# Optimization experiments

Measured on AMD Instinct MI355X. Metric: run time of the kernel, lower is better.

## Reference

```python
import jax, jax.numpy as jnp
import numpy as np

N, T, D, C = 32, 512, 1024, 120
EPS = 1e-12
SCALE = 2.0 * (D ** 0.5)


def setup_inputs() -> dict:
    key = jax.random.key(0)
    ks = jax.random.split(key, 16)
    inp = {
        'anc_perm_input': jax.random.normal(ks[0], (N, T, D), dtype=jnp.float32),
        'pos_perm_input': jax.random.normal(ks[1], (N, T, D), dtype=jnp.float32),
        'neg_perm_input': jax.random.normal(ks[2], (N, T, D), dtype=jnp.float32),
        'anc_src_key_padding_mask': jax.random.randint(ks[3], (N, T), 0, 2) == 1,
        'pos_src_key_padding_mask': jax.random.randint(ks[4], (N, T), 0, 2) == 1,
        'neg_src_key_padding_mask': jax.random.randint(ks[5], (N, T), 0, 2) == 1,
        # learned parameters (stored as (in, out); math-equivalent to torch x @ W.T)
        'W_attn': jax.random.normal(ks[6], (D, D), dtype=jnp.float32) * 0.02,
        'b_attn': jnp.zeros((D,), dtype=jnp.float32),
        'W1': jax.random.normal(ks[7], (D, D), dtype=jnp.float32) * 0.02,
        'b1': jnp.zeros((D,), dtype=jnp.float32),
        'W2': jax.random.normal(ks[8], (D, D), dtype=jnp.float32) * 0.02,
        'b2': jnp.zeros((D,), dtype=jnp.float32),
        'ln_g': jnp.ones((D,), dtype=jnp.float32),
        'ln_b': jnp.zeros((D,), dtype=jnp.float32),
        'W_last': jax.random.normal(ks[9], (D, C), dtype=jnp.float32) * 0.02,
        'b_last': jnp.zeros((C,), dtype=jnp.float32),
    }
    return inp


def _ntd_nd(x, mask, W_attn, b_attn, W1, b1, W2, b2, ln_g, ln_b, W_last, b_last):
    # x: (N,T,D); mask: (N,T) bool, True = padding
    w = x @ W_attn + b_attn                                   # (N,T,D)
    valid = ~mask                                             # (N,T)
    scores = jnp.einsum('btd,bsd->bts', w, w)                 # (N,T,T)
    scores = jnp.where(valid[:, :, None] & valid[:, None, :], scores, 0.0)
    s = jnp.sum(scores, axis=1) / SCALE                       # (N,T)
    s = jnp.where(mask, -jnp.inf, s)
    attn = jax.nn.softmax(s, axis=1)                          # (N,T)
    # proj_head: duplicate OrderedDict key => linear1 -> relu -> linear2 (no final act)
    proj = jax.nn.relu(x @ W1 + b1) @ W2 + b2                 # (N,T,D)
    pooled = jnp.einsum('bt,btd->bd', attn, proj)             # (N,D)
    mu = jnp.mean(pooled, axis=-1, keepdims=True)
    var = jnp.var(pooled, axis=-1, keepdims=True)
    normed = (pooled - mu) / jnp.sqrt(var + EPS) * ln_g + ln_b
    return jax.nn.relu(normed) @ W_last + b_last              # (N,C)


def reference(anc_perm_input, pos_perm_input, neg_perm_input,
              anc_src_key_padding_mask, pos_src_key_padding_mask, neg_src_key_padding_mask,
              W_attn, b_attn, W1, b1, W2, b2, ln_g, ln_b, W_last, b_last):
    params = (W_attn, b_attn, W1, b1, W2, b2, ln_g, ln_b, W_last, b_last)
    anc = _ntd_nd(anc_perm_input, anc_src_key_padding_mask, *params)
    pos = _ntd_nd(pos_perm_input, pos_src_key_padding_mask, *params)
    neg = _ntd_nd(neg_perm_input, neg_src_key_padding_mask, *params)
    return (anc, pos, neg)
```

## Files before the change

### kernel.cpp

```cpp
#include <hip/hip_runtime.h>
#include <hip/hip_bf16.h>
#include <math.h>

#define N_B 32
#define T_S 512
#define D_D 1024
#define C_C 120
#define ZB 96
#define SCALE 64.0f

typedef unsigned short u16;
typedef __attribute__((ext_vector_type(8))) short short8;
typedef __attribute__((ext_vector_type(8))) unsigned short ushort8;
typedef __attribute__((ext_vector_type(4))) float floatx4;

__device__ inline u16 f2bf(float f) {
    union { __hip_bfloat16 h; u16 u; } c; c.h = __float2bfloat16(f); return c.u;
}
__device__ inline float bf2f(u16 u) {
    union { unsigned i; float f; } c; c.i = ((unsigned)u) << 16; return c.f;
}

__device__ inline void gll16(const void* g, void* l) {
    __builtin_amdgcn_global_load_lds((const __attribute__((address_space(1))) void*)g,
                                     (__attribute__((address_space(3))) void*)l,
                                     16, 0, 0);
}

__device__ inline bool mask_is_i8(const int* mk) {
    bool i8 = false;
#pragma unroll
    for (int i = 0; i < 16; i++) {
        unsigned v = ((const unsigned*)mk)[i];
        if (v > 1u) i8 = true;
    }
    return i8;
}
__device__ inline int mask_val(const int* mk, int idx, bool i8) {
    return i8 ? (int)((const signed char*)mk)[idx] : mk[idx];
}

__global__ __launch_bounds__(512)
void k_scan(const int* m0, const int* m1, const int* m2,
            int* __restrict__ slotbase, int* __restrict__ cnts,
            int* __restrict__ gb, int* __restrict__ zblk,
            int* __restrict__ mtot, u16* __restrict__ xp,
            float* __restrict__ attnw, float4* __restrict__ zreg) {
    int zb = blockIdx.x;
    int tid = threadIdx.x;
    {
        float4 zz4 = {0.f, 0.f, 0.f, 0.f};
        for (int i = zb * 512 + tid; i < (2 * 1024 * 1024 / 16); i += ZB * 512)
            zreg[i] = zz4;
    }
    bool i8_0 = mask_is_i8(m0), i8_1 = mask_is_i8(m1), i8_2 = mask_is_i8(m2);
    __shared__ unsigned short wc[ZB][8];
    __shared__ int scnt[ZB], sgb[ZB], stot;
    int wave = tid >> 6, lane = tid & 63;
#pragma unroll
    for (int it = 0; it < 12; it++) {
        int zb2 = wave * 12 + it;
        int z2 = zb2 >> 5, b2 = zb2 & 31;
        const int* mk = z2 == 0 ? m0 : (z2 == 1 ? m1 : m2);
        bool i8 = z2 == 0 ? i8_0 : (z2 == 1 ? i8_1 : i8_2);
        int c = 0;
        if (i8) {
            const signed char* p = (const signed char*)mk + b2 * T_S + lane * 8;
#pragma unroll
            for (int e = 0; e < 8; e++) c += (p[e] == 0);
        } else {
            const int* p = mk + b2 * T_S + lane * 8;
#pragma unroll
            for (int e = 0; e < 8; e++) c += (p[e] == 0);
        }
        c += __shfl_xor(c, 1, 64);
        c += __shfl_xor(c, 2, 64);
        c += __shfl_xor(c, 4, 64);
        if ((lane & 7) == 0) wc[zb2][lane >> 3] = (unsigned short)c;
    }
    __syncthreads();
    if (tid < ZB) {
        int s = 0;
#pragma unroll
        for (int c = 0; c < 8; c++) s += wc[tid][c];
        scnt[tid] = s;
    }
    __syncthreads();
    if (tid == 0) {
        int run = 0;
        for (int i = 0; i < ZB; i++) { sgb[i] = run; run += (scnt[i] + 63) & ~63; }
        stot = run;
    }
    __syncthreads();
    int cnt = scnt[zb], base = sgb[zb];
    if (tid == 0) {
        cnts[zb] = cnt; gb[zb] = base;
        int run = base;
#pragma unroll
        for (int c = 0; c < 8; c++) { slotbase[zb * 8 + c] = run; run += wc[zb][c]; }
        if (zb == ZB - 1) mtot[0] = stot;
    }
    int nb = (cnt + 63) >> 6;
    if (tid < nb) zblk[(base >> 6) + tid] = zb;
    int cend = (cnt + 63) & ~63;
    {
        u16* bp = xp + (size_t)(base + cnt) * D_D;
        int n8 = (cend - cnt) * (D_D / 8);
        ushort8 zz = {0,0,0,0,0,0,0,0};
        for (int i = tid; i < n8; i += 512)
            *(ushort8*)(bp + (size_t)i * 8) = zz;
    }
    if (zb == ZB - 1) {
        int tot = stot, tend = (tot + 255) & ~255;
        u16* bp = xp + (size_t)tot * D_D;
        int n8 = (tend - tot) * (D_D / 8);
        ushort8 zz = {0,0,0,0,0,0,0,0};
        for (int i = tid; i < n8; i += 512)
            *(ushort8*)(bp + (size_t)i * 8) = zz;
        for (int i = tid; i < tend - tot; i += 512) attnw[tot + i] = 0.f;
        if (tid < ((tend - tot) >> 6)) zblk[(tot >> 6) + tid] = 0;
    }
}

__global__ void k_prep(const float* __restrict__ W_attn, const float* __restrict__ W1,
                       const float* x0, const float* x1, const float* x2,
                       const int* m0, const int* m1, const int* m2,
                       const int* __restrict__ slotbase,
                       float* __restrict__ WT, u16* __restrict__ W1T,
                       float* __restrict__ xsum, u16* __restrict__ xp) {
    int bx = blockIdx.x;
    int tid = threadIdx.x;
    if (bx < 1024) {
        int tbx = bx & 31, tby = bx >> 5;
        __shared__ float tile[32][33];
        int tx = tid & 31, ty = tid >> 5;
#pragma unroll
        for (int j = 0; j < 32; j += 8)
            tile[ty + j][tx] = W_attn[(size_t)(tby*32 + ty + j)*D_D + tbx*32 + tx];
        __syncthreads();
#pragma unroll
        for (int j = 0; j < 32; j += 8)
            WT[(size_t)(tbx*32 + ty + j)*D_D + tby*32 + tx] = tile[tx][ty + j];
        __syncthreads();
#pragma unroll
        for (int j = 0; j < 32; j += 8)
            tile[ty + j][tx] = W1[(size_t)(tby*32 + ty + j)*D_D + tbx*32 + tx];
        __syncthreads();
#pragma unroll
        for (int j = 0; j < 32; j += 8)
            W1T[(size_t)(tbx*32 + ty + j)*D_D + tby*32 + tx] = f2bf(tile[tx][ty + j]);
        return;
    }
    int idx = bx - 1024;
    int chunk = idx & 7, zb = idx >> 3;
    int z = zb >> 5, b = zb & 31;
    const float* x = z == 0 ? x0 : (z == 1 ? x1 : x2);
    const int* mk = z == 0 ? m0 : (z == 1 ? m1 : m2);
    bool i8 = mask_is_i8(mk);
    int t0 = chunk * 64;
    __shared__ unsigned char s_list[64];
    __shared__ int s_cc;
    if (tid < 64) {
        bool v = (mask_val(mk, b * T_S + t0 + tid, i8) == 0);
        unsigned long long bal = __ballot(v);
        int pos = (int)__popcll(bal & ((1ull << tid) - 1ull));
        if (v) s_list[pos] = (unsigned char)tid;
        if (tid == 0) s_cc = (int)__popcll(bal);
    }
    __syncthreads();
    int cc = s_cc;
    int slot0 = slotbase[zb * 8 + chunk];
    const float4* xr = (const float4*)(x + (size_t)(b * T_S) * D_D);
    float4 acc = {0.f, 0.f, 0.f, 0.f};
#pragma unroll 2
    for (int j = 0; j < cc; j++) {
        int t = t0 + (int)s_list[j];
        float4 v = xr[(size_t)t * 256 + tid];
        union { __hip_bfloat162 h; ushort2 u; } c0, c1;
        c0.h = __float22bfloat162_rn({v.x, v.y});
        c1.h = __float22bfloat162_rn({v.z, v.w});
        ushort4 uu = {c0.u.x, c0.u.y, c1.u.x, c1.u.y};
        *(ushort4*)(xp + (size_t)(slot0 + j) * D_D + tid * 4) = uu;
        acc.x += v.x; acc.y += v.y; acc.z += v.z; acc.w += v.w;
    }
    float* xs = xsum + (size_t)zb * D_D + tid * 4;
    atomicAdd(xs + 0, acc.x); atomicAdd(xs + 1, acc.y);
    atomicAdd(xs + 2, acc.z); atomicAdd(xs + 3, acc.w);
}

__global__ void k_matvec(const float* __restrict__ W, const float* __restrict__ vin,
                         const float* __restrict__ bias, const int* __restrict__ bmul,
                         float scale, float* __restrict__ vout) {
    int z = blockIdx.z, bg = blockIdx.y;
    int och = blockIdx.x >> 3, kc = blockIdx.x & 7;
    int o = och * 256 + threadIdx.x;
    int brow = z * N_B + bg * 4;
    float acc[4] = {0.f, 0.f, 0.f, 0.f};
    if (kc == 0 && bias) {
        float bv = bias[o];
#pragma unroll
        for (int bb = 0; bb < 4; bb++)
            acc[bb] = bmul ? bv * (float)bmul[brow + bb] : bv;
    }
    const float* vi = vin + (size_t)brow * D_D + kc * 128;
    const float* Wp = W + (size_t)(kc * 128) * D_D + o;
#pragma unroll 4
    for (int i = 0; i < 128; i++) {
        float wv = Wp[(size_t)i * D_D];
#pragma unroll
        for (int bb = 0; bb < 4; bb++)
            acc[bb] += vi[(size_t)bb * D_D + i] * wv;
    }
#pragma unroll
    for (int bb = 0; bb < 4; bb++)
        atomicAdd(&vout[(size_t)(brow + bb) * D_D + o], acc[bb] * scale);
}

__global__ void k_dots(const u16* __restrict__ xp, const float* __restrict__ vs,
                       const int* __restrict__ zblk, const int* __restrict__ mtot,
                       float* __restrict__ sdot) {
    int t0 = blockIdx.x * 4;
    if (t0 >= mtot[0]) return;
    int t = t0 + (threadIdx.x >> 6);
    int lane = threadIdx.x & 63;
    int zb = zblk[t0 >> 6];
    const u16* xr = xp + (size_t)t * D_D;
    const float* vr = vs + (size_t)zb * D_D;
    float acc = 0.f;
#pragma unroll
    for (int i = 0; i < 2; i++) {
        short8 v = *(const short8*)(xr + i * 512 + lane * 8);
        const float* vp = vr + i * 512 + lane * 8;
        float4 a0 = *(const float4*)(vp);
        float4 a1 = *(const float4*)(vp + 4);
        acc += bf2f((u16)v[0]) * a0.x + bf2f((u16)v[1]) * a0.y
             + bf2f((u16)v[2]) * a0.z + bf2f((u16)v[3]) * a0.w
             + bf2f((u16)v[4]) * a1.x + bf2f((u16)v[5]) * a1.y
             + bf2f((u16)v[6]) * a1.z + bf2f((u16)v[7]) * a1.w;
    }
#pragma unroll
    for (int off = 32; off; off >>= 1) acc += __shfl_xor(acc, off, 64);
    if (lane == 0) sdot[t] = acc;
}

__global__ void k_smax(const float* __restrict__ sdot, const int* __restrict__ cnts,
                       const int* __restrict__ gb, float* __restrict__ attnw) {
    int zb = blockIdx.x, tid = threadIdx.x;
    __shared__ float redm[8], reds[8];
    int cnt = cnts[zb], base = gb[zb];
    int wave = tid >> 6, lane = tid & 63;
    float v = (tid < cnt) ? sdot[base + tid] : -INFINITY;
    float mx = v;
#pragma unroll
    for (int off = 32; off; off >>= 1) mx = fmaxf(mx, __shfl_xor(mx, off, 64));
    if (lane == 0) redm[wave] = mx;
    __syncthreads();
    mx = redm[0];
#pragma unroll
    for (int k = 1; k < 8; k++) mx = fmaxf(mx, redm[k]);
    float e = __expf(v - mx);
    float es = e;
#pragma unroll
    for (int off = 32; off; off >>= 1) es += __shfl_xor(es, off, 64);
    if (lane == 0) reds[wave] = es;
    __syncthreads();
    float tot = 0.f;
#pragma unroll
    for (int k = 0; k < 8; k++) tot += reds[k];
    int cend = (cnt + 63) & ~63;
    if (tid < cend) attnw[base + tid] = (tid < cnt) ? (e / tot) : 0.f;
}

#define STAGE_TILE(buf, k0)                                                   \
    {                                                                         \
        _Pragma("unroll")                                                     \
        for (int i_ = 0; i_ < 4; i_++) {                                      \
            int r0_ = i_ * 64 + wave * 8;                                     \
            int rr_ = r0_ + srow;                                             \
            int gc_ = cp ^ srow;            \
            gll16(abase + (size_t)rr_ * D_D + (k0) + gc_ * 8,                 \
                  &As[buf][r0_ * 64]);                                        \
            gll16(bbase + (size_t)rr_ * D_D + (k0) + gc_ * 8,                 \
                  &Bs[buf][r0_ * 64]);                                        \
        }                                                                     \
    }

__global__ __launch_bounds__(512, 1)
void k_gemm_bf16(const u16* __restrict__ xp, const u16* __restrict__ W1T,
                 const float* __restrict__ b1, const float* __restrict__ attnw,
                 const int* __restrict__ zblk, const int* __restrict__ mtot,
                 float* __restrict__ rbuf) {
    int bid = blockIdx.x;
    int sub = bid & 31;
    int Mt = (bid >> 5) * 8 + (sub & 7);
    int Nt = sub >> 3;
    int row0 = Mt * 256, N0 = Nt * 256;
    if (row0 >= mtot[0]) return;

    __shared__ __align__(16) u16 As[2][256 * 64];
    __shared__ __align__(16) u16 Bs[2][256 * 64];
    __shared__ float sAttn[256];
    int tid = threadIdx.x;
    int wave = tid >> 6, lane = tid & 63;
    if (tid < 256) sAttn[tid] = attnw[row0 + tid];

    int wy = wave >> 2, wx = wave & 3;
    int q = lane >> 4, cidx = lane & 15;
    int srow = lane >> 3;
    int cp = lane & 7;

    floatx4 acc[8][4];
#pragma unroll
    for (int mi = 0; mi < 8; mi++)
#pragma unroll
        for (int ni = 0; ni < 4; ni++)
            acc[mi][ni] = (floatx4){0.f, 0.f, 0.f, 0.f};

    const u16* abase = xp + (size_t)row0 * D_D;
    const u16* bbase = W1T + (size_t)N0 * D_D;

    STAGE_TILE(0, 0)
    __syncthreads();
    int cur = 0;
#pragma unroll 2
    for (int kt = 0; kt < 16; kt++) {
        if (kt < 15) { STAGE_TILE(cur ^ 1, (kt + 1) << 6) }
        __builtin_amdgcn_sched_barrier(0);
#pragma unroll
        for (int ks = 0; ks < 2; ks++) {
            short8 a[8], bfr[4];
#pragma unroll
            for (int mi = 0; mi < 8; mi++) {
                int m = wy * 128 + mi * 16 + cidx;
                a[mi] = *(const short8*)&As[cur][m * 64 + ((((ks << 2) | q) ^ (m & 7)) << 3)];
            }
#pragma unroll
            for (int ni = 0; ni < 4; ni++) {
                int n = wx * 64 + ni * 16 + cidx;
                bfr[ni] = *(const short8*)&Bs[cur][n * 64 + ((((ks << 2) | q) ^ (n & 7)) << 3)];
            }
#pragma unroll
            for (int mi = 0; mi < 8; mi++)
#pragma unroll
                for (int ni = 0; ni < 4; ni++)
                    acc[mi][ni] = __builtin_amdgcn_mfma_f32_16x16x32_bf16(
                        a[mi], bfr[ni], acc[mi][ni], 0, 0, 0);
        }
        __syncthreads();
        cur ^= 1;
    }

    int zb0 = zblk[(row0 >> 6) + wy * 2];
    int zb1 = zblk[(row0 >> 6) + wy * 2 + 1];
#pragma unroll
    for (int ni = 0; ni < 4; ni++) {
        int ng = N0 + wx * 64 + ni * 16 + cidx;
        float b1v = b1[ng];
        float s0 = 0.f, s1 = 0.f;
#pragma unroll
        for (int mi = 0; mi < 8; mi++) {
            float part = 0.f;
#pragma unroll
            for (int rg = 0; rg < 4; rg++) {
                int ml = wy * 128 + mi * 16 + q * 4 + rg;
                float hv = fmaxf(acc[mi][ni][rg] + b1v, 0.f);
                part += hv * sAttn[ml];
            }
            if (mi < 4) s0 += part; else s1 += part;
        }
        s0 += __shfl_xor(s0, 16, 64); s0 += __shfl_xor(s0, 32, 64);
        s1 += __shfl_xor(s1, 16, 64); s1 += __shfl_xor(s1, 32, 64);
        if (lane < 16) {
            atomicAdd(&rbuf[(size_t)zb0 * D_D + ng], s0);
            atomicAdd(&rbuf[(size_t)zb1 * D_D + ng], s1);
        }
    }
}

__global__ void k_fin(const float* __restrict__ pooled, const float* __restrict__ ln_g,
                      const float* __restrict__ ln_b, const float* __restrict__ Wl,
                      const float* __restrict__ bl, float* __restrict__ out) {
    int zb = blockIdx.x;
    int tid = threadIdx.x;
    __shared__ float nr[D_D];
    __shared__ float redA[8], redB[8];
    __shared__ float ps[4][C_C];
    const float* p = pooled + (size_t)zb * D_D;
    int o0 = tid, o1 = tid + 512;
    float a0 = p[o0], a1 = p[o1];
    float s1 = a0 + a1, s2 = a0 * a0 + a1 * a1;
#pragma unroll
    for (int off = 32; off; off >>= 1) {
        s1 += __shfl_xor(s1, off, 64);
        s2 += __shfl_xor(s2, off, 64);
    }
    int w = tid >> 6;
    if ((tid & 63) == 0) { redA[w] = s1; redB[w] = s2; }
    __syncthreads();
    float t1 = 0.f, t2 = 0.f;
#pragma unroll
    for (int k = 0; k < 8; k++) { t1 += redA[k]; t2 += redB[k]; }
    float mu = t1 * (1.0f / D_D);
    float var = t2 * (1.0f / D_D) - mu * mu;
    float rstd = 1.0f / sqrtf(var + 1e-12f);
    nr[o0] = fmaxf((a0 - mu) * rstd * ln_g[o0] + ln_b[o0], 0.f);
    nr[o1] = fmaxf((a1 - mu) * rstd * ln_g[o1] + ln_b[o1], 0.f);
    __syncthreads();
    if (tid < 4 * C_C) {
        int seg = tid / C_C, c = tid - seg * C_C;
        const float* wp = Wl + (size_t)(seg * 256) * C_C + c;
        const float* np = nr + seg * 256;
        float acc = 0.f;
#pragma unroll 8
        for (int d = 0; d < 256; d++)
            acc += np[d] * wp[(size_t)d * C_C];
        ps[seg][c] = acc;
    }
    __syncthreads();
    if (tid < C_C)
        out[(size_t)zb * C_C + tid] =
            bl[tid] + ps[0][tid] + ps[1][tid] + ps[2][tid] + ps[3][tid];
}

extern "C" void kernel_launch(void* const* d_in, const int* in_sizes, int n_in,
                              void* d_out, int out_size, void* d_ws, size_t ws_size,
                              hipStream_t stream) {
    const float* x0 = (const float*)d_in[0];
    const float* x1 = (const float*)d_in[1];
    const float* x2 = (const float*)d_in[2];
    const int* m0 = (const int*)d_in[3];
    const int* m1 = (const int*)d_in[4];
    const int* m2 = (const int*)d_in[5];
    const float* W_attn = (const float*)d_in[6];
    const float* b_attn = (const float*)d_in[7];
    const float* W1 = (const float*)d_in[8];
    const float* b1 = (const float*)d_in[9];
    const float* W2 = (const float*)d_in[10];
    const float* b2 = (const float*)d_in[11];
    const float* ln_g = (const float*)d_in[12];
    const float* ln_b = (const float*)d_in[13];
    const float* W_last = (const float*)d_in[14];
    const float* b_last = (const float*)d_in[15];
    float* out = (float*)d_out;

    char* wsb = (char*)d_ws;
    const size_t MB = 1 << 20;
    float* WT     = (float*)(wsb);
    u16*   W1T    = (u16*)  (wsb + 4 * MB);
    float* xsum   = (float*)(wsb + 6 * MB);
    float* rbuf   = (float*)(wsb + 6 * MB + 393216);
    float* wsum   = (float*)(wsb + 6 * MB + 786432);
    float* vs     = (float*)(wsb + 6 * MB + 1179648);
    float* pooled = (float*)(wsb + 6 * MB + 1572864);
    float* sdot   = (float*)(wsb + 8 * MB);
    float* attnw  = (float*)(wsb + 8 * MB + 262144);
    int*   slotb  = (int*)  (wsb + 8 * MB + 524288);
    int*   cnts   = (int*)  (wsb + 8 * MB + 528384);
    int*   gb     = (int*)  (wsb + 8 * MB + 532480);
    int*   mtot   = (int*)  (wsb + 8 * MB + 536576);
    int*   zblk   = (int*)  (wsb + 8 * MB + 540672);
    u16*   xp     = (u16*)  (wsb + 9 * MB);

    k_scan  <<<ZB, 512, 0, stream>>>(m0, m1, m2, slotb, cnts, gb, zblk, mtot,
                                     xp, attnw, (float4*)(wsb + 6 * MB));
    k_prep  <<<1792, 256, 0, stream>>>(W_attn, W1, x0, x1, x2, m0, m1, m2,
                                       slotb, WT, W1T, xsum, xp);
    k_matvec<<<dim3(32, 8, 3), 256, 0, stream>>>(W_attn, xsum, b_attn, cnts, 1.0f, wsum);
    k_matvec<<<dim3(32, 8, 3), 256, 0, stream>>>(WT, wsum, nullptr, nullptr, 1.0f / SCALE, vs);
    k_dots  <<<12288, 256, 0, stream>>>(xp, vs, zblk, mtot, sdot);
    k_smax  <<<ZB, 512, 0, stream>>>(sdot, cnts, gb, attnw);
    k_gemm_bf16<<<768, 512, 0, stream>>>(xp, W1T, b1, attnw, zblk, mtot, rbuf);
    k_matvec<<<dim3(32, 8, 3), 256, 0, stream>>>(W2, rbuf, b2, nullptr, 1.0f, pooled);
    k_fin   <<<ZB, 512, 0, stream>>>(pooled, ln_g, ln_b, W_last, b_last, out);
}
```

Before: 370.1 us.

## Widen prep copy vectors, batch matvec rows, and reuse vector in dots kernel

The prep kernel now has each thread move 8 contiguous elements and handle two rows per iteration, using 16-byte bf16 stores. The matvec kernel processes 8 batch rows per block instead of 4, so each weight load is reused twice as often and the grid is halved. The dots kernel keeps the per-segment vector in registers and loops over 64 rows per block instead of 4, cutting redundant vector loads and block count. The cost is fewer blocks, which lowers parallelism, and more registers per thread.

```diff
diff --git a/kernel.cpp b/kernel.cpp
--- a/kernel.cpp
+++ b/kernel.cpp
@@ -171,21 +171,32 @@
     int cc = s_cc;
     int slot0 = slotbase[zb * 8 + chunk];
     const float4* xr = (const float4*)(x + (size_t)(b * T_S) * D_D);
-    float4 acc = {0.f, 0.f, 0.f, 0.f};
-#pragma unroll 2
-    for (int j = 0; j < cc; j++) {
-        int t = t0 + (int)s_list[j];
-        float4 v = xr[(size_t)t * 256 + tid];
-        union { __hip_bfloat162 h; ushort2 u; } c0, c1;
-        c0.h = __float22bfloat162_rn({v.x, v.y});
-        c1.h = __float22bfloat162_rn({v.z, v.w});
-        ushort4 uu = {c0.u.x, c0.u.y, c1.u.x, c1.u.y};
-        *(ushort4*)(xp + (size_t)(slot0 + j) * D_D + tid * 4) = uu;
-        acc.x += v.x; acc.y += v.y; acc.z += v.z; acc.w += v.w;
-    }
-    float* xs = xsum + (size_t)zb * D_D + tid * 4;
-    atomicAdd(xs + 0, acc.x); atomicAdd(xs + 1, acc.y);
-    atomicAdd(xs + 2, acc.z); atomicAdd(xs + 3, acc.w);
+    int half = tid >> 7;
+    int c128 = tid & 127;
+    float4 a0s = {0.f, 0.f, 0.f, 0.f}, a1s = {0.f, 0.f, 0.f, 0.f};
+    for (int j = 0; j < cc; j += 2) {
+        int jr = j + half;
+        if (jr < cc) {
+            int t = t0 + (int)s_list[jr];
+            float4 v0 = xr[(size_t)t * 256 + c128 * 2];
+            float4 v1 = xr[(size_t)t * 256 + c128 * 2 + 1];
+            union { __hip_bfloat162 h; ushort2 u; } c0, c1, c2, c3;
+            c0.h = __float22bfloat162_rn({v0.x, v0.y});
+            c1.h = __float22bfloat162_rn({v0.z, v0.w});
+            c2.h = __float22bfloat162_rn({v1.x, v1.y});
+            c3.h = __float22bfloat162_rn({v1.z, v1.w});
+            ushort8 uu = {c0.u.x, c0.u.y, c1.u.x, c1.u.y,
+                          c2.u.x, c2.u.y, c3.u.x, c3.u.y};
+            *(ushort8*)(xp + (size_t)(slot0 + jr) * D_D + c128 * 8) = uu;
+            a0s.x += v0.x; a0s.y += v0.y; a0s.z += v0.z; a0s.w += v0.w;
+            a1s.x += v1.x; a1s.y += v1.y; a1s.z += v1.z; a1s.w += v1.w;
+        }
+    }
+    float* xs = xsum + (size_t)zb * D_D + c128 * 8;
+    atomicAdd(xs + 0, a0s.x); atomicAdd(xs + 1, a0s.y);
+    atomicAdd(xs + 2, a0s.z); atomicAdd(xs + 3, a0s.w);
+    atomicAdd(xs + 4, a1s.x); atomicAdd(xs + 5, a1s.y);
+    atomicAdd(xs + 6, a1s.z); atomicAdd(xs + 7, a1s.w);
 }
 
 __global__ void k_matvec(const float* __restrict__ W, const float* __restrict__ vin,
@@ -194,12 +205,12 @@
     int z = blockIdx.z, bg = blockIdx.y;
     int och = blockIdx.x >> 3, kc = blockIdx.x & 7;
     int o = och * 256 + threadIdx.x;
-    int brow = z * N_B + bg * 4;
-    float acc[4] = {0.f, 0.f, 0.f, 0.f};
+    int brow = z * N_B + bg * 8;
+    float acc[8] = {0.f, 0.f, 0.f, 0.f, 0.f, 0.f, 0.f, 0.f};
     if (kc == 0 && bias) {
         float bv = bias[o];
 #pragma unroll
-        for (int bb = 0; bb < 4; bb++)
+        for (int bb = 0; bb < 8; bb++)
             acc[bb] = bmul ? bv * (float)bmul[brow + bb] : bv;
     }
     const float* vi = vin + (size_t)brow * D_D + kc * 128;
@@ -208,39 +219,48 @@
     for (int i = 0; i < 128; i++) {
         float wv = Wp[(size_t)i * D_D];
 #pragma unroll
-        for (int bb = 0; bb < 4; bb++)
+        for (int bb = 0; bb < 8; bb++)
             acc[bb] += vi[(size_t)bb * D_D + i] * wv;
     }
 #pragma unroll
-    for (int bb = 0; bb < 4; bb++)
+    for (int bb = 0; bb < 8; bb++)
         atomicAdd(&vout[(size_t)(brow + bb) * D_D + o], acc[bb] * scale);
 }
 
 __global__ void k_dots(const u16* __restrict__ xp, const float* __restrict__ vs,
                        const int* __restrict__ zblk, const int* __restrict__ mtot,
                        float* __restrict__ sdot) {
-    int t0 = blockIdx.x * 4;
+    int g = blockIdx.x;
+    int t0 = g * 64;
     if (t0 >= mtot[0]) return;
-    int t = t0 + (threadIdx.x >> 6);
-    int lane = threadIdx.x & 63;
-    int zb = zblk[t0 >> 6];
-    const u16* xr = xp + (size_t)t * D_D;
+    int wave = threadIdx.x >> 6, lane = threadIdx.x & 63;
+    int zb = zblk[g];
     const float* vr = vs + (size_t)zb * D_D;
-    float acc = 0.f;
-#pragma unroll
-    for (int i = 0; i < 2; i++) {
-        short8 v = *(const short8*)(xr + i * 512 + lane * 8);
-        const float* vp = vr + i * 512 + lane * 8;
-        float4 a0 = *(const float4*)(vp);
-        float4 a1 = *(const float4*)(vp + 4);
-        acc += bf2f((u16)v[0]) * a0.x + bf2f((u16)v[1]) * a0.y
-             + bf2f((u16)v[2]) * a0.z + bf2f((u16)v[3]) * a0.w
-             + bf2f((u16)v[4]) * a1.x + bf2f((u16)v[5]) * a1.y
-             + bf2f((u16)v[6]) * a1.z + bf2f((u16)v[7]) * a1.w;
-    }
-#pragma unroll
-    for (int off = 32; off; off >>= 1) acc += __shfl_xor(acc, off, 64);
-    if (lane == 0) sdot[t] = acc;
+    float vreg[16];
+    {
+        float4 a0 = *(const float4*)(vr + lane * 8);
+        float4 a1 = *(const float4*)(vr + lane * 8 + 4);
+        float4 a2 = *(const float4*)(vr + 512 + lane * 8);
+        float4 a3 = *(const float4*)(vr + 512 + lane * 8 + 4);
+        vreg[0]=a0.x; vreg[1]=a0.y; vreg[2]=a0.z; vreg[3]=a0.w;
+        vreg[4]=a1.x; vreg[5]=a1.y; vreg[6]=a1.z; vreg[7]=a1.w;
+        vreg[8]=a2.x; vreg[9]=a2.y; vreg[10]=a2.z; vreg[11]=a2.w;
+        vreg[12]=a3.x; vreg[13]=a3.y; vreg[14]=a3.z; vreg[15]=a3.w;
+    }
+#pragma unroll 4
+    for (int r = wave; r < 64; r += 4) {
+        const u16* xr = xp + (size_t)(t0 + r) * D_D;
+        short8 v0 = *(const short8*)(xr + lane * 8);
+        short8 v1 = *(const short8*)(xr + 512 + lane * 8);
+        float acc = 0.f;
+#pragma unroll
+        for (int e = 0; e < 8; e++) acc += bf2f((u16)v0[e]) * vreg[e];
+#pragma unroll
+        for (int e = 0; e < 8; e++) acc += bf2f((u16)v1[e]) * vreg[e + 8];
+#pragma unroll
+        for (int off = 32; off; off >>= 1) acc += __shfl_xor(acc, off, 64);
+        if (lane == 0) sdot[t0 + r] = acc;
+    }
 }
 
 __global__ void k_smax(const float* __restrict__ sdot, const int* __restrict__ cnts,
@@ -465,11 +485,11 @@
                                      xp, attnw, (float4*)(wsb + 6 * MB));
     k_prep  <<<1792, 256, 0, stream>>>(W_attn, W1, x0, x1, x2, m0, m1, m2,
                                        slotb, WT, W1T, xsum, xp);
-    k_matvec<<<dim3(32, 8, 3), 256, 0, stream>>>(W_attn, xsum, b_attn, cnts, 1.0f, wsum);
-    k_matvec<<<dim3(32, 8, 3), 256, 0, stream>>>(WT, wsum, nullptr, nullptr, 1.0f / SCALE, vs);
-    k_dots  <<<12288, 256, 0, stream>>>(xp, vs, zblk, mtot, sdot);
+    k_matvec<<<dim3(32, 4, 3), 256, 0, stream>>>(W_attn, xsum, b_attn, cnts, 1.0f, wsum);
+    k_matvec<<<dim3(32, 4, 3), 256, 0, stream>>>(WT, wsum, nullptr, nullptr, 1.0f / SCALE, vs);
+    k_dots  <<<768, 256, 0, stream>>>(xp, vs, zblk, mtot, sdot);
     k_smax  <<<ZB, 512, 0, stream>>>(sdot, cnts, gb, attnw);
     k_gemm_bf16<<<768, 512, 0, stream>>>(xp, W1T, b1, attnw, zblk, mtot, rbuf);
-    k_matvec<<<dim3(32, 8, 3), 256, 0, stream>>>(W2, rbuf, b2, nullptr, 1.0f, pooled);
+    k_matvec<<<dim3(32, 4, 3), 256, 0, stream>>>(W2, rbuf, b2, nullptr, 1.0f, pooled);
     k_fin   <<<ZB, 512, 0, stream>>>(pooled, ln_g, ln_b, W_last, b_last, out);
 }
```

Measured after the change: 395.2 us. 6.8% more time.
